# Performance work log

Measured on AMD Instinct MI355X. Metric: run time of the kernel, lower is better.

The kernel has to match this reference:

```python
import jax, jax.numpy as jnp
import numpy as np

NUM_GROUPS = 32
EPS = 1e-5

def group_norm(x, gamma, beta):
    # x: [B, C, L]
    B, C, L = x.shape
    g = x.reshape(B, NUM_GROUPS, C // NUM_GROUPS, L)
    mu = g.mean(axis=(2, 3), keepdims=True)
    var = g.var(axis=(2, 3), keepdims=True)
    g = (g - mu) * jax.lax.rsqrt(var + EPS)
    h = g.reshape(B, C, L)
    return h * gamma[None, :, None] + beta[None, :, None]

def conv1x1(h, W, b):
    # h: [B, C, L], W: [Cout, Cin], b: [Cout] -> [B, Cout, L]
    return jnp.einsum('oc,bcl->bol', W, h) + b[None, :, None]

def setup_inputs() -> dict:
    key = jax.random.key(0)
    ks = jax.random.split(key, 10)
    B, C, L = 8, 512, 2048
    s = 1.0 / np.sqrt(C)
    inp = {
        'x': jax.random.normal(ks[0], (B, C, L), dtype=jnp.float32),
        'gn_gamma': jnp.ones((C,), jnp.float32),
        'gn_beta': jnp.zeros((C,), jnp.float32),
        'Wq': jax.random.normal(ks[1], (C, C), jnp.float32) * s,
        'bq': jnp.zeros((C,), jnp.float32),
        'Wk': jax.random.normal(ks[2], (C, C), jnp.float32) * s,
        'bk': jnp.zeros((C,), jnp.float32),
        'Wv': jax.random.normal(ks[3], (C, C), jnp.float32) * s,
        'bv': jnp.zeros((C,), jnp.float32),
        'Wo': jax.random.normal(ks[4], (C, C), jnp.float32) * s,
        'bo': jnp.zeros((C,), jnp.float32),
    }
    return inp

def reference(x, gn_gamma, gn_beta, Wq, bq, Wk, bk, Wv, bv, Wo, bo):
    B, C, L = x.shape
    h = group_norm(x, gn_gamma, gn_beta)
    q = conv1x1(h, Wq, bq)  # [B, C, L]
    k = conv1x1(h, Wk, bk)  # [B, C, L]
    v = conv1x1(h, Wv, bv)  # [B, C, L]
    scale = 1.0 / jnp.sqrt(jnp.float32(C)).astype(x.dtype)
    w = jnp.einsum('bci,bcj->bij', q, k) * scale  # [B, L, L]
    w = jax.nn.softmax(w, axis=-1)
    a = jnp.einsum('bij,bcj->bci', w, v)  # [B, C, L]
    return x + conv1x1(a, Wo, bo)
```

## Files before the change

kernel.cpp:

```cpp
#include <hip/hip_runtime.h>
#include <hip/hip_bf16.h>

#define B_ 8
#define C_ 512
#define L_ 2048
#define G_ 32

typedef __attribute__((ext_vector_type(8))) short bf16x8;
typedef __attribute__((ext_vector_type(4))) float f32x4;

__device__ __forceinline__ float b2f(short h) {
    union { unsigned u; float f; } c; c.u = ((unsigned)(unsigned short)h) << 16; return c.f;
}
__device__ __forceinline__ short f2b(float f) {
    union { float f; unsigned u; } c; c.f = f;
    unsigned r = (c.u + 0x7FFFu + ((c.u >> 16) & 1u)) >> 16;
    return (short)r;
}

__device__ __forceinline__ void load_lds16(const void* g, void* s) {
    __builtin_amdgcn_global_load_lds(
        (const __attribute__((address_space(1))) void*)g,
        (__attribute__((address_space(3))) void*)s, 16, 0, 0);
}

template<int N>
__device__ __forceinline__ void wait_vm() {
    if constexpr (N == 0)      asm volatile("s_waitcnt vmcnt(0)" ::: "memory");
    else if constexpr (N == 6) asm volatile("s_waitcnt vmcnt(6)" ::: "memory");
    else                       asm volatile("s_waitcnt vmcnt(8)" ::: "memory");
    __builtin_amdgcn_sched_barrier(0);
}
__device__ __forceinline__ void sbar() {
    __builtin_amdgcn_sched_barrier(0);
    __builtin_amdgcn_s_barrier();
    __builtin_amdgcn_sched_barrier(0);
}

__global__ __launch_bounds__(256) void cvt_w(
    const float* __restrict__ a, const float* __restrict__ b,
    const float* __restrict__ c, const float* __restrict__ d,
    short* __restrict__ o)
{
    const float* src = (blockIdx.y == 0) ? a : (blockIdx.y == 1) ? b
                     : (blockIdx.y == 2) ? c : d;
    short* dst = o + (size_t)blockIdx.y * (C_ * C_);
    int i = (blockIdx.x * 256 + threadIdx.x) * 4;
    float4 v = *(const float4*)(src + i);
    short4 r;
    r.x = f2b(v.x); r.y = f2b(v.y); r.z = f2b(v.z); r.w = f2b(v.w);
    *(short4*)(dst + i) = r;
}

__global__ __launch_bounds__(256) void groupnorm_tr(
    const float* __restrict__ x, const float* __restrict__ gamma,
    const float* __restrict__ beta, short* __restrict__ h_t,
    float* __restrict__ rsum)
{
    int bg = blockIdx.x;
    int b = bg >> 5, g = bg & 31;
    const float* xg = x + ((size_t)b * C_ + (size_t)g * 16) * L_;
    int t = threadIdx.x;
    if (t < 64) rsum[(size_t)bg * 64 + t] = 0.f;
    float s = 0.f, ss = 0.f;
    for (int i = t; i < 8192; i += 256) {
        float4 v = ((const float4*)xg)[i];
        s  += v.x + v.y + v.z + v.w;
        ss += v.x * v.x + v.y * v.y + v.z * v.z + v.w * v.w;
    }
    #pragma unroll
    for (int o = 32; o > 0; o >>= 1) { s += __shfl_down(s, o); ss += __shfl_down(ss, o); }
    __shared__ float rs[4], rss[4], stats[2], gam[16], bet[16];
    int wave = t >> 6, lane = t & 63;
    if (lane == 0) { rs[wave] = s; rss[wave] = ss; }
    if (t < 16) { gam[t] = gamma[g * 16 + t]; bet[t] = beta[g * 16 + t]; }
    __syncthreads();
    if (t == 0) {
        float S = rs[0] + rs[1] + rs[2] + rs[3];
        float SS = rss[0] + rss[1] + rss[2] + rss[3];
        float mean = S * (1.f / 32768.f);
        float var = SS * (1.f / 32768.f) - mean * mean;
        stats[0] = mean; stats[1] = rsqrtf(var + 1e-5f);
    }
    __syncthreads();
    float mean = stats[0], rstd = stats[1];
    short* ho = h_t + (size_t)b * L_ * C_ + (size_t)g * 16;
    for (int i = t; i < 32768; i += 256) {
        int cl = i & 15, l = i >> 4;
        float xv = xg[cl * L_ + l];
        float hv = (xv - mean) * rstd * gam[cl] + bet[cl];
        ho[(size_t)l * C_ + cl] = f2b(hv);
    }
}

template<int BM, int PIPE, int BIAS_MODE, bool RESID, bool OUTF32, bool EXPSUM, bool ROWDIV>
__global__ __launch_bounds__(BM * 2) void gemm_bt(
    const short* __restrict__ A, const short* __restrict__ Bt,
    void* __restrict__ Co, const float* __restrict__ bias,
    const float* __restrict__ bias2, const float* __restrict__ resid,
    float* __restrict__ rowsum,
    int N, int K, int lda, int ldb, int ldc,
    long sA, long sB, long sC, float alpha)
{
    constexpr int T = BM * 2;
    constexpr int RPP = T / 8;
    constexpr int LPS = BM / RPP + 128 / RPP;
    constexpr int NBUF = (PIPE == 1) ? 2 : 1;
    __shared__ __align__(16) short As[NBUF][BM * 64];
    __shared__ __align__(16) short Bs[NBUF][128 * 64];

    int nbx = gridDim.x, nby = gridDim.y, nbz = gridDim.z;
    int lin = blockIdx.x + nbx * (blockIdx.y + nby * blockIdx.z);
    int total = nbx * nby * nbz;
    int bx, by, bz;
    if ((total & 7) == 0) {
        int chunk = total >> 3;
        int logical = (lin & 7) * chunk + (lin >> 3);
        bx = logical % nbx; int t2 = logical / nbx; by = t2 % nby; bz = t2 / nby;
    } else { bx = blockIdx.x; by = blockIdx.y; bz = blockIdx.z; }

    const short* Ab = A + (size_t)bz * sA;
    const short* Bb = Bt + (size_t)bz * sB;
    int m0 = by * BM, n0 = bx * 128;
    int t = threadIdx.x, lane = t & 63;
    int wave = t >> 6;
    int wm = wave >> 1, wn = wave & 1;

    f32x4 acc[4][4] = {};

    int rs_ = t >> 3, cs_ = t & 7;
    int gcol = ((cs_ ^ (rs_ & 7)) << 3);
    const short* gA = Ab + (size_t)(m0 + rs_) * lda + gcol;
    const short* gB = Bb + (size_t)(n0 + rs_) * ldb + gcol;
    int fr = lane & 15, fq = lane >> 4;
    int ch0 = (fq ^ (fr & 7)) << 3;
    int ch1 = ((4 | fq) ^ (fr & 7)) << 3;

    auto stage = [&](short* Asb, short* Bsb) {
        #pragma unroll
        for (int i = 0; i < BM / RPP; i++)
            load_lds16(gA + (size_t)(RPP * i) * lda, Asb + i * (RPP * 64) + t * 8);
        #pragma unroll
        for (int i = 0; i < 128 / RPP; i++)
            load_lds16(gB + (size_t)(RPP * i) * ldb, Bsb + i * (RPP * 64) + t * 8);
        gA += 64; gB += 64;
    };
    auto compute = [&](const short* Asb, const short* Bsb) {
        #pragma unroll
        for (int kk = 0; kk < 2; kk++) {
            int ch = kk ? ch1 : ch0;
            bf16x8 af[4], bfr[4];
            #pragma unroll
            for (int i = 0; i < 4; i++) {
                int R = wm * 64 + i * 16 + fr;
                af[i] = *(const bf16x8*)(Asb + R * 64 + ch);
            }
            #pragma unroll
            for (int j = 0; j < 4; j++) {
                int R = wn * 64 + j * 16 + fr;
                bfr[j] = *(const bf16x8*)(Bsb + R * 64 + ch);
            }
            #pragma unroll
            for (int mt = 0; mt < 4; mt++)
                #pragma unroll
                for (int nt = 0; nt < 4; nt++)
                    acc[mt][nt] = __builtin_amdgcn_mfma_f32_16x16x32_bf16(
                        af[mt], bfr[nt], acc[mt][nt], 0, 0, 0);
        }
    };

    if constexpr (PIPE == 0) {
        for (int k0 = 0; k0 < K; k0 += 64) {
            __syncthreads();
            stage(As[0], Bs[0]);
            __syncthreads();
            compute(As[0], Bs[0]);
        }
    } else {
        int nk = K >> 6;
        stage(As[0], Bs[0]);
        stage(As[1], Bs[1]);
        wait_vm<LPS>();
        sbar();
        for (int kt = 0; kt < nk; kt += 2) {
            compute(As[0], Bs[0]);
            sbar();
            if (kt + 2 < nk) { stage(As[0], Bs[0]); wait_vm<LPS>(); }
            else               wait_vm<0>();
            sbar();
            compute(As[1], Bs[1]);
            sbar();
            if (kt + 3 < nk) { stage(As[1], Bs[1]); wait_vm<LPS>(); }
            else               wait_vm<0>();
            sbar();
        }
    }

    size_t cb = (size_t)bz * sC;
    int crow = (lane >> 4) * 4;
    int wrow = wm * 64;
    float psum[4][4];
    float inv[4][4];
    if (EXPSUM) {
        #pragma unroll
        for (int mt = 0; mt < 4; mt++)
            #pragma unroll
            for (int r = 0; r < 4; r++) psum[mt][r] = 0.f;
    }
    if (ROWDIV) {
        #pragma unroll
        for (int mt = 0; mt < 4; mt++)
            #pragma unroll
            for (int r = 0; r < 4; r++) {
                int m = m0 + wrow + mt * 16 + crow + r;
                inv[mt][r] = 1.f / rowsum[(size_t)bz * L_ + m];
            }
    }
    #pragma unroll
    for (int mt = 0; mt < 4; mt++) {
        #pragma unroll
        for (int nt = 0; nt < 4; nt++) {
            int n = n0 + wn * 64 + nt * 16 + fr;
            float bn = 0.f;
            if (BIAS_MODE == 3) bn = (n < 512) ? bias[n] : bias2[n - 512];
            #pragma unroll
            for (int r = 0; r < 4; r++) {
                int m = m0 + wrow + mt * 16 + crow + r;
                float v = acc[mt][nt][r] * alpha;
                if (EXPSUM) { v = __expf(v); psum[mt][r] += v; }
                if (ROWDIV) v *= inv[mt][r];
                if (BIAS_MODE == 3) v += bn;
                if (BIAS_MODE == 2) v += bias[m];
                size_t idx = cb + (size_t)m * ldc + n;
                if (RESID) v += resid[idx];
                if (OUTF32) ((float*)Co)[idx] = v;
                else        ((short*)Co)[idx] = f2b(v);
            }
        }
    }
    if (EXPSUM) {
        #pragma unroll
        for (int mt = 0; mt < 4; mt++)
            #pragma unroll
            for (int r = 0; r < 4; r++) {
                float s = psum[mt][r];
                s += __shfl_xor(s, 1); s += __shfl_xor(s, 2);
                s += __shfl_xor(s, 4); s += __shfl_xor(s, 8);
                if ((lane & 15) == 0) {
                    int m = m0 + wrow + mt * 16 + crow + r;
                    atomicAdd(rowsum + (size_t)bz * L_ + m, s);
                }
            }
    }
}

extern "C" void kernel_launch(void* const* d_in, const int* in_sizes, int n_in,
                              void* d_out, int out_size, void* d_ws, size_t ws_size,
                              hipStream_t stream)
{
    const float* x     = (const float*)d_in[0];
    const float* gamma = (const float*)d_in[1];
    const float* beta  = (const float*)d_in[2];
    const float* Wq    = (const float*)d_in[3];
    const float* bq    = (const float*)d_in[4];
    const float* Wk    = (const float*)d_in[5];
    const float* bk    = (const float*)d_in[6];
    const float* Wv    = (const float*)d_in[7];
    const float* bv    = (const float*)d_in[8];
    const float* Wo    = (const float*)d_in[9];
    const float* bo    = (const float*)d_in[10];
    float* out = (float*)d_out;

    const size_t MiB = 1024 * 1024;
    const size_t CC = (size_t)C_ * C_;
    const size_t LC = (size_t)L_ * C_;
    const size_t LL = (size_t)L_ * L_;
    const size_t wbytes = 4 * CC * sizeof(short);

    const size_t perb = 16 * MiB + L_ * sizeof(float);
    int nb = 1;
    for (int c = 8; c >= 1; c >>= 1)
        if (ws_size >= wbytes + (size_t)c * perb) { nb = c; break; }

    short* wq_b = (short*)d_ws;
    short* wv_b = wq_b + 2 * CC;
    short* wo_b = wv_b + CC;
    short* h_t  = wo_b + CC;
    short* qk_t = h_t + (size_t)nb * LC;
    short* v_   = qk_t + (size_t)nb * 2 * LC;
    short* S    = v_  + (size_t)nb * LC;
    float* rsum = (float*)(S + (size_t)nb * LL);
    short* a_t  = h_t;

    const long sLC = (long)LC;
    const long sLL = (long)LL;
    const float scale = 0.044194173824159216f;

    cvt_w<<<dim3(C_ * C_ / 1024, 4), 256, 0, stream>>>(Wq, Wk, Wv, Wo, wq_b);

    for (int b0 = 0; b0 < B_; b0 += nb) {
        const float* xb = x + (size_t)b0 * LC;
        float* outb = out + (size_t)b0 * LC;

        groupnorm_tr<<<dim3(nb * G_), 256, 0, stream>>>(xb, gamma, beta, h_t, rsum);

        gemm_bt<128, 1, 3, false, false, false, false><<<dim3(8, 16, nb), 256, 0, stream>>>(
            h_t, wq_b, qk_t, bq, bk, nullptr, nullptr,
            1024, 512, 512, 512, 1024, sLC, 0, 2 * sLC, 1.f);
        gemm_bt<128, 1, 2, false, false, false, false><<<dim3(16, 4, nb), 256, 0, stream>>>(
            wv_b, h_t, v_, bv, nullptr, nullptr, nullptr,
            2048, 512, 512, 512, 2048, 0, sLC, sLC, 1.f);
        gemm_bt<256, 0, 0, false, false, true, false><<<dim3(16, 8, nb), 512, 0, stream>>>(
            qk_t, qk_t + 512, S, nullptr, nullptr, nullptr, rsum,
            2048, 512, 1024, 1024, 2048, 2 * sLC, 2 * sLC, sLL, scale);
        gemm_bt<128, 1, 0, false, false, false, true><<<dim3(4, 16, nb), 256, 0, stream>>>(
            S, v_, a_t, nullptr, nullptr, nullptr, rsum,
            512, 2048, 2048, 2048, 512, sLL, sLC, sLC, 1.f);
        gemm_bt<128, 1, 2, true, true, false, false><<<dim3(16, 4, nb), 256, 0, stream>>>(
            wo_b, a_t, outb, bo, nullptr, xb, nullptr,
            2048, 512, 512, 512, 2048, 0, sLC, sLC, 1.f);
    }
}
```

Baseline: 303.7 us.

## Add 256x256 8-wave pipelined GEMM kernel for QK projection and scores

Adds a new gemm8 kernel with 256x256 tiles, 8 waves, double-buffered LDS staging interleaved with MFMA sub-blocks, setprio hints and an XCD-aware block remap. It replaces the generic gemm_bt for the fused Q/K projection and for the QK^T score GEMM with fused exp and row-sum. The goal is more reuse per tile and better overlap of global-to-LDS loads with matrix math. The cost is higher register and LDS pressure (128KB LDS per block) and fewer blocks for the smaller projection GEMM.

Result: no change. 300.3 us (-1.1%).

```diff
diff --git a/kernel.cpp b/kernel.cpp
--- a/kernel.cpp
+++ b/kernel.cpp
@@ -27,8 +27,13 @@
 template<int N>
 __device__ __forceinline__ void wait_vm() {
     if constexpr (N == 0)      asm volatile("s_waitcnt vmcnt(0)" ::: "memory");
+    else if constexpr (N == 2) asm volatile("s_waitcnt vmcnt(2)" ::: "memory");
     else if constexpr (N == 6) asm volatile("s_waitcnt vmcnt(6)" ::: "memory");
     else                       asm volatile("s_waitcnt vmcnt(8)" ::: "memory");
+    __builtin_amdgcn_sched_barrier(0);
+}
+__device__ __forceinline__ void wait_lgkm0() {
+    asm volatile("s_waitcnt lgkmcnt(0)" ::: "memory");
     __builtin_amdgcn_sched_barrier(0);
 }
 __device__ __forceinline__ void sbar() {
@@ -90,6 +95,157 @@
         float xv = xg[cl * L_ + l];
         float hv = (xv - mean) * rstd * gam[cl] + bet[cl];
         ho[(size_t)l * C_ + cl] = f2b(hv);
+    }
+}
+
+#define MM(mh, nh, bfx)                                                        \
+  do {                                                                         \
+    _Pragma("unroll") for (int i_ = 0; i_ < 4; i_++)                           \
+    _Pragma("unroll") for (int j_ = 0; j_ < 2; j_++)                           \
+    _Pragma("unroll") for (int kk_ = 0; kk_ < 2; kk_++)                        \
+      acc[(mh)*4 + i_][(nh)*2 + j_] = __builtin_amdgcn_mfma_f32_16x16x32_bf16( \
+          af[i_][kk_], bfx[j_][kk_], acc[(mh)*4 + i_][(nh)*2 + j_], 0, 0, 0);  \
+  } while (0)
+
+template<int BIAS_MODE, bool EXPSUM>
+__global__ __launch_bounds__(512, 2) void gemm8(
+    const short* __restrict__ A, const short* __restrict__ Bt,
+    void* __restrict__ Co, const float* __restrict__ bias,
+    const float* __restrict__ bias2, float* __restrict__ rowsum,
+    int K, int lda, int ldb, int ldc,
+    long sA, long sB, long sC, float alpha)
+{
+    __shared__ __align__(16) short As0[256 * 64];
+    __shared__ __align__(16) short As1[256 * 64];
+    __shared__ __align__(16) short Bs0[256 * 64];
+    __shared__ __align__(16) short Bs1[256 * 64];
+
+    int nbx = gridDim.x, nby = gridDim.y, nbz = gridDim.z;
+    int lin = blockIdx.x + nbx * (blockIdx.y + nby * blockIdx.z);
+    int total = nbx * nby * nbz;
+    int bx, by, bz;
+    if ((total & 7) == 0) {
+        int chunk = total >> 3;
+        int logical = (lin & 7) * chunk + (lin >> 3);
+        bx = logical % nbx; int t2 = logical / nbx; by = t2 % nby; bz = t2 / nby;
+    } else { bx = blockIdx.x; by = blockIdx.y; bz = blockIdx.z; }
+
+    int m0 = by * 256, n0 = bx * 256;
+    int t = threadIdx.x, lane = t & 63;
+    int wave = t >> 6;
+    int wm = wave >> 2, wn = wave & 3;
+    int fr = lane & 15, fq = lane >> 4;
+    int ch0 = (fq ^ (fr & 7)) << 3;
+    int ch1 = ((4 | fq) ^ (fr & 7)) << 3;
+    int rs_ = t >> 3, cs_ = t & 7;
+    int gcol = ((cs_ ^ (rs_ & 7)) << 3);
+
+    const short* gA = A + (size_t)bz * sA + (size_t)(m0 + rs_) * lda + gcol;
+    const short* gB = Bt + (size_t)bz * sB + (size_t)(n0 + rs_) * ldb + gcol;
+
+    f32x4 acc[8][4] = {};
+    bf16x8 af[4][2], bf0[2][2], bf1[2][2];
+
+    auto stgA = [&](short* dst, int tile, int h) {
+        const short* s = gA + (size_t)(h * 128) * lda + tile * 64;
+        load_lds16(s, dst + h * 8192 + t * 8);
+        load_lds16(s + (size_t)64 * lda, dst + h * 8192 + 4096 + t * 8);
+    };
+    auto stgB = [&](short* dst, int tile, int h) {
+        const short* s = gB + (size_t)(h * 128) * ldb + tile * 64;
+        load_lds16(s, dst + h * 8192 + t * 8);
+        load_lds16(s + (size_t)64 * ldb, dst + h * 8192 + 4096 + t * 8);
+    };
+    auto rdA = [&](const short* S, int mh) {
+        #pragma unroll
+        for (int i = 0; i < 4; i++) {
+            int R = wm * 128 + (mh * 4 + i) * 16 + fr;
+            af[i][0] = *(const bf16x8*)(S + R * 64 + ch0);
+            af[i][1] = *(const bf16x8*)(S + R * 64 + ch1);
+        }
+    };
+    auto rdB = [&](const short* S, int nh, bf16x8 (&bf)[2][2]) {
+        #pragma unroll
+        for (int j = 0; j < 2; j++) {
+            int R = wn * 64 + (nh * 2 + j) * 16 + fr;
+            bf[j][0] = *(const bf16x8*)(S + R * 64 + ch0);
+            bf[j][1] = *(const bf16x8*)(S + R * 64 + ch1);
+        }
+    };
+
+    int nk = K >> 6;
+
+    auto TILE = [&](short* cA, short* cB, short* nA, short* nB, int tt) {
+        rdA(cA, 0); rdB(cB, 0, bf0);
+        if (tt + 1 < nk) stgA(nA, tt + 1, 1);
+        sbar(); wait_lgkm0();
+        __builtin_amdgcn_s_setprio(1); MM(0, 0, bf0); __builtin_amdgcn_s_setprio(0);
+        sbar();
+        rdB(cB, 1, bf1);
+        if (tt + 1 < nk) stgB(nB, tt + 1, 0);
+        sbar(); wait_lgkm0();
+        __builtin_amdgcn_s_setprio(1); MM(0, 1, bf1); __builtin_amdgcn_s_setprio(0);
+        sbar();
+        rdA(cA, 1);
+        if (tt + 1 < nk) stgB(nB, tt + 1, 1);
+        sbar(); wait_lgkm0();
+        __builtin_amdgcn_s_setprio(1); MM(1, 0, bf0); __builtin_amdgcn_s_setprio(0);
+        sbar();
+        if (tt + 2 < nk) stgA(cA, tt + 2, 0);
+        __builtin_amdgcn_s_setprio(1); MM(1, 1, bf1); __builtin_amdgcn_s_setprio(0);
+        if (tt + 2 < nk) wait_vm<2>(); else wait_vm<0>();
+        sbar();
+    };
+
+    stgA(As0, 0, 0); stgA(As0, 0, 1); stgB(Bs0, 0, 0); stgB(Bs0, 0, 1);
+    if (nk > 1) stgA(As1, 1, 0);
+    wait_vm<2>();
+    sbar();
+
+    for (int tt = 0; tt < nk; tt += 2) {
+        TILE(As0, Bs0, As1, Bs1, tt);
+        TILE(As1, Bs1, As0, Bs0, tt + 1);
+    }
+
+    size_t cb = (size_t)bz * sC;
+    int crow = fq * 4;
+    float psum[8][4];
+    if (EXPSUM) {
+        #pragma unroll
+        for (int mi = 0; mi < 8; mi++)
+            #pragma unroll
+            for (int r = 0; r < 4; r++) psum[mi][r] = 0.f;
+    }
+    #pragma unroll
+    for (int mi = 0; mi < 8; mi++) {
+        #pragma unroll
+        for (int nj = 0; nj < 4; nj++) {
+            int n = n0 + wn * 64 + nj * 16 + fr;
+            float bn = 0.f;
+            if (BIAS_MODE == 3) bn = (n < 512) ? bias[n] : bias2[n - 512];
+            #pragma unroll
+            for (int r = 0; r < 4; r++) {
+                int m = m0 + wm * 128 + mi * 16 + crow + r;
+                float v = acc[mi][nj][r] * alpha;
+                if (EXPSUM) { v = __expf(v); psum[mi][r] += v; }
+                if (BIAS_MODE == 3) v += bn;
+                ((short*)Co)[cb + (size_t)m * ldc + n] = f2b(v);
+            }
+        }
+    }
+    if (EXPSUM) {
+        #pragma unroll
+        for (int mi = 0; mi < 8; mi++)
+            #pragma unroll
+            for (int r = 0; r < 4; r++) {
+                float s = psum[mi][r];
+                s += __shfl_xor(s, 1); s += __shfl_xor(s, 2);
+                s += __shfl_xor(s, 4); s += __shfl_xor(s, 8);
+                if ((lane & 15) == 0) {
+                    int m = m0 + wm * 128 + mi * 16 + crow + r;
+                    atomicAdd(rowsum + (size_t)bz * L_ + m, s);
+                }
+            }
     }
 }
 
@@ -304,15 +460,15 @@
 
         groupnorm_tr<<<dim3(nb * G_), 256, 0, stream>>>(xb, gamma, beta, h_t, rsum);
 
-        gemm_bt<128, 1, 3, false, false, false, false><<<dim3(8, 16, nb), 256, 0, stream>>>(
-            h_t, wq_b, qk_t, bq, bk, nullptr, nullptr,
-            1024, 512, 512, 512, 1024, sLC, 0, 2 * sLC, 1.f);
+        gemm8<3, false><<<dim3(4, 8, nb), 512, 0, stream>>>(
+            h_t, wq_b, qk_t, bq, bk, nullptr,
+            512, 512, 512, 1024, sLC, 0, 2 * sLC, 1.f);
         gemm_bt<128, 1, 2, false, false, false, false><<<dim3(16, 4, nb), 256, 0, stream>>>(
             wv_b, h_t, v_, bv, nullptr, nullptr, nullptr,
             2048, 512, 512, 512, 2048, 0, sLC, sLC, 1.f);
-        gemm_bt<256, 0, 0, false, false, true, false><<<dim3(16, 8, nb), 512, 0, stream>>>(
-            qk_t, qk_t + 512, S, nullptr, nullptr, nullptr, rsum,
-            2048, 512, 1024, 1024, 2048, 2 * sLC, 2 * sLC, sLL, scale);
+        gemm8<0, true><<<dim3(8, 8, nb), 512, 0, stream>>>(
+            qk_t, qk_t + 512, S, nullptr, nullptr, rsum,
+            512, 1024, 1024, 2048, 2 * sLC, 2 * sLC, sLL, scale);
         gemm_bt<128, 1, 0, false, false, false, true><<<dim3(4, 16, nb), 256, 0, stream>>>(
             S, v_, a_t, nullptr, nullptr, nullptr, rsum,
             512, 2048, 2048, 2048, 512, sLL, sLC, sLC, 1.f);
```

## Fuse QK^T scores and V projection into one launch, stage groupnorm via LDS

Applied to the files above, without the earlier changes.

The QK^T score GEMM (with exp and row-sum) and the V projection GEMM now run as tiles of a single kernel launch, with an interleaved block-to-tile mapping. This removes one launch and lets the two independent GEMMs fill the device together. Groupnorm now caches the group's input in shared memory during the statistics pass, so the second pass reads LDS instead of re-reading global memory, and it writes packed bf16 pairs. The exp uses exp2 with a pre-folded log2e scale, and the Q/K projection switches to 256-row tiles without double buffering, which may lower occupancy or overlap.

New measurement: 275.7 us. -9.2%, faster.

```diff
diff --git a/kernel.cpp b/kernel.cpp
--- a/kernel.cpp
+++ b/kernel.cpp
@@ -9,9 +9,6 @@
 typedef __attribute__((ext_vector_type(8))) short bf16x8;
 typedef __attribute__((ext_vector_type(4))) float f32x4;
 
-__device__ __forceinline__ float b2f(short h) {
-    union { unsigned u; float f; } c; c.u = ((unsigned)(unsigned short)h) << 16; return c.f;
-}
 __device__ __forceinline__ short f2b(float f) {
     union { float f; unsigned u; } c; c.f = f;
     unsigned r = (c.u + 0x7FFFu + ((c.u >> 16) & 1u)) >> 16;
@@ -27,7 +24,6 @@
 template<int N>
 __device__ __forceinline__ void wait_vm() {
     if constexpr (N == 0)      asm volatile("s_waitcnt vmcnt(0)" ::: "memory");
-    else if constexpr (N == 6) asm volatile("s_waitcnt vmcnt(6)" ::: "memory");
     else                       asm volatile("s_waitcnt vmcnt(8)" ::: "memory");
     __builtin_amdgcn_sched_barrier(0);
 }
@@ -57,20 +53,24 @@
     const float* __restrict__ beta, short* __restrict__ h_t,
     float* __restrict__ rsum)
 {
+    __shared__ float xb[16][2052];
+    __shared__ float rs[4], rss[4], stats[2], gam[16], bet[16];
     int bg = blockIdx.x;
     int b = bg >> 5, g = bg & 31;
     const float* xg = x + ((size_t)b * C_ + (size_t)g * 16) * L_;
     int t = threadIdx.x;
     if (t < 64) rsum[(size_t)bg * 64 + t] = 0.f;
     float s = 0.f, ss = 0.f;
+    #pragma unroll 4
     for (int i = t; i < 8192; i += 256) {
         float4 v = ((const float4*)xg)[i];
+        int cl = i >> 9, l4 = (i & 511) << 2;
+        *(float4*)&xb[cl][l4] = v;
         s  += v.x + v.y + v.z + v.w;
         ss += v.x * v.x + v.y * v.y + v.z * v.z + v.w * v.w;
     }
     #pragma unroll
     for (int o = 32; o > 0; o >>= 1) { s += __shfl_down(s, o); ss += __shfl_down(ss, o); }
-    __shared__ float rs[4], rss[4], stats[2], gam[16], bet[16];
     int wave = t >> 6, lane = t & 63;
     if (lane == 0) { rs[wave] = s; rss[wave] = ss; }
     if (t < 16) { gam[t] = gamma[g * 16 + t]; bet[t] = beta[g * 16 + t]; }
@@ -85,15 +85,135 @@
     __syncthreads();
     float mean = stats[0], rstd = stats[1];
     short* ho = h_t + (size_t)b * L_ * C_ + (size_t)g * 16;
-    for (int i = t; i < 32768; i += 256) {
-        int cl = i & 15, l = i >> 4;
-        float xv = xg[cl * L_ + l];
-        float hv = (xv - mean) * rstd * gam[cl] + bet[cl];
-        ho[(size_t)l * C_ + cl] = f2b(hv);
-    }
-}
-
-template<int BM, int PIPE, int BIAS_MODE, bool RESID, bool OUTF32, bool EXPSUM, bool ROWDIV>
+    for (int i = t; i < 16384; i += 256) {
+        int cp = (i & 7) * 2, l = i >> 3;
+        float a0 = (xb[cp][l]     - mean) * rstd * gam[cp]     + bet[cp];
+        float a1 = (xb[cp + 1][l] - mean) * rstd * gam[cp + 1] + bet[cp + 1];
+        unsigned pk = (unsigned)(unsigned short)f2b(a0)
+                    | ((unsigned)(unsigned short)f2b(a1) << 16);
+        *(unsigned*)(ho + (size_t)l * C_ + cp) = pk;
+    }
+}
+
+__global__ __launch_bounds__(512) void qk_vproj(
+    const short* __restrict__ qk, const short* __restrict__ ht,
+    const short* __restrict__ wv, short* __restrict__ S,
+    short* __restrict__ v_, const float* __restrict__ bv,
+    float* __restrict__ rsum, int nb, float alpha2)
+{
+    __shared__ __align__(16) short As[256 * 64];
+    __shared__ __align__(16) short Bs[128 * 64];
+    const int LC = L_ * C_;
+    const size_t LL = (size_t)L_ * L_;
+
+    int total = nb * 160;
+    int lin = blockIdx.x;
+    int chunk = total >> 3;
+    int logical = (lin & 7) * chunk + (lin >> 3);
+    int qkN = nb << 7;
+    bool isQK = logical < qkN;
+    int bz, bx, by;
+    if (isQK) { bz = logical >> 7; int rr = logical & 127; bx = rr & 15; by = rr >> 4; }
+    else      { int r = logical - qkN; bz = r >> 5; int rr = r & 31; bx = rr & 15; by = rr >> 4; }
+
+    int m0 = by * 256, n0 = bx * 128;
+    int lda = isQK ? 1024 : 512;
+    const short* Ab = isQK ? qk + (size_t)bz * (2 * LC) : wv;
+    const short* Bb = isQK ? qk + 512 + (size_t)bz * (2 * LC) : ht + (size_t)bz * LC;
+
+    int t = threadIdx.x, lane = t & 63, wave = t >> 6;
+    int wm = wave >> 1, wn = wave & 1;
+    f32x4 acc[4][4] = {};
+
+    int rs_ = t >> 3, cs_ = t & 7;
+    int gcol = (cs_ ^ (rs_ & 7)) << 3;
+    const short* gA = Ab + (size_t)(m0 + rs_) * lda + gcol;
+    const short* gB = Bb + (size_t)(n0 + rs_) * lda + gcol;
+    int fr = lane & 15, fq = lane >> 4;
+    int ch0 = (fq ^ (fr & 7)) << 3, ch1 = ((4 | fq) ^ (fr & 7)) << 3;
+
+    for (int k0 = 0; k0 < 512; k0 += 64) {
+        __syncthreads();
+        #pragma unroll
+        for (int i = 0; i < 4; i++)
+            load_lds16(gA + (size_t)(64 * i) * lda, As + i * 4096 + t * 8);
+        #pragma unroll
+        for (int i = 0; i < 2; i++)
+            load_lds16(gB + (size_t)(64 * i) * lda, Bs + i * 4096 + t * 8);
+        gA += 64; gB += 64;
+        __syncthreads();
+        #pragma unroll
+        for (int kk = 0; kk < 2; kk++) {
+            int ch = kk ? ch1 : ch0;
+            bf16x8 af[4], bfr[4];
+            #pragma unroll
+            for (int i = 0; i < 4; i++)
+                af[i] = *(const bf16x8*)(As + (wm * 64 + i * 16 + fr) * 64 + ch);
+            #pragma unroll
+            for (int j = 0; j < 4; j++)
+                bfr[j] = *(const bf16x8*)(Bs + (wn * 64 + j * 16 + fr) * 64 + ch);
+            #pragma unroll
+            for (int mt = 0; mt < 4; mt++)
+                #pragma unroll
+                for (int nt = 0; nt < 4; nt++)
+                    acc[mt][nt] = __builtin_amdgcn_mfma_f32_16x16x32_bf16(
+                        af[mt], bfr[nt], acc[mt][nt], 0, 0, 0);
+        }
+    }
+
+    int crow = fq * 4, wrow = wm * 64;
+    if (isQK) {
+        short* Co = S + (size_t)bz * LL;
+        float psum[4][4];
+        #pragma unroll
+        for (int mt = 0; mt < 4; mt++)
+            #pragma unroll
+            for (int r = 0; r < 4; r++) psum[mt][r] = 0.f;
+        #pragma unroll
+        for (int mt = 0; mt < 4; mt++) {
+            #pragma unroll
+            for (int nt = 0; nt < 4; nt++) {
+                int n = n0 + wn * 64 + nt * 16 + fr;
+                #pragma unroll
+                for (int r = 0; r < 4; r++) {
+                    int m = m0 + wrow + mt * 16 + crow + r;
+                    float v = exp2f(acc[mt][nt][r] * alpha2);
+                    psum[mt][r] += v;
+                    Co[(size_t)m * L_ + n] = f2b(v);
+                }
+            }
+        }
+        #pragma unroll
+        for (int mt = 0; mt < 4; mt++)
+            #pragma unroll
+            for (int r = 0; r < 4; r++) {
+                float s = psum[mt][r];
+                s += __shfl_xor(s, 1); s += __shfl_xor(s, 2);
+                s += __shfl_xor(s, 4); s += __shfl_xor(s, 8);
+                if ((lane & 15) == 0) {
+                    int m = m0 + wrow + mt * 16 + crow + r;
+                    atomicAdd(rsum + (size_t)bz * L_ + m, s);
+                }
+            }
+    } else {
+        short* Co = v_ + (size_t)bz * LC;
+        #pragma unroll
+        for (int mt = 0; mt < 4; mt++) {
+            #pragma unroll
+            for (int nt = 0; nt < 4; nt++) {
+                int n = n0 + wn * 64 + nt * 16 + fr;
+                #pragma unroll
+                for (int r = 0; r < 4; r++) {
+                    int m = m0 + wrow + mt * 16 + crow + r;
+                    float v = acc[mt][nt][r] + bv[m];
+                    Co[(size_t)m * L_ + n] = f2b(v);
+                }
+            }
+        }
+    }
+}
+
+template<int BM, int PIPE, int BIAS_MODE, bool RESID, bool OUTF32, bool ROWDIV>
 __global__ __launch_bounds__(BM * 2) void gemm_bt(
     const short* __restrict__ A, const short* __restrict__ Bt,
     void* __restrict__ Co, const float* __restrict__ bias,
@@ -151,15 +271,11 @@
             int ch = kk ? ch1 : ch0;
             bf16x8 af[4], bfr[4];
             #pragma unroll
-            for (int i = 0; i < 4; i++) {
-                int R = wm * 64 + i * 16 + fr;
-                af[i] = *(const bf16x8*)(Asb + R * 64 + ch);
-            }
-            #pragma unroll
-            for (int j = 0; j < 4; j++) {
-                int R = wn * 64 + j * 16 + fr;
-                bfr[j] = *(const bf16x8*)(Bsb + R * 64 + ch);
-            }
+            for (int i = 0; i < 4; i++)
+                af[i] = *(const bf16x8*)(Asb + (wm * 64 + i * 16 + fr) * 64 + ch);
+            #pragma unroll
+            for (int j = 0; j < 4; j++)
+                bfr[j] = *(const bf16x8*)(Bsb + (wn * 64 + j * 16 + fr) * 64 + ch);
             #pragma unroll
             for (int mt = 0; mt < 4; mt++)
                 #pragma unroll
@@ -199,14 +315,7 @@
     size_t cb = (size_t)bz * sC;
     int crow = (lane >> 4) * 4;
     int wrow = wm * 64;
-    float psum[4][4];
     float inv[4][4];
-    if (EXPSUM) {
-        #pragma unroll
-        for (int mt = 0; mt < 4; mt++)
-            #pragma unroll
-            for (int r = 0; r < 4; r++) psum[mt][r] = 0.f;
-    }
     if (ROWDIV) {
         #pragma unroll
         for (int mt = 0; mt < 4; mt++)
@@ -227,7 +336,6 @@
             for (int r = 0; r < 4; r++) {
                 int m = m0 + wrow + mt * 16 + crow + r;
                 float v = acc[mt][nt][r] * alpha;
-                if (EXPSUM) { v = __expf(v); psum[mt][r] += v; }
                 if (ROWDIV) v *= inv[mt][r];
                 if (BIAS_MODE == 3) v += bn;
                 if (BIAS_MODE == 2) v += bias[m];
@@ -237,20 +345,6 @@
                 else        ((short*)Co)[idx] = f2b(v);
             }
         }
-    }
-    if (EXPSUM) {
-        #pragma unroll
-        for (int mt = 0; mt < 4; mt++)
-            #pragma unroll
-            for (int r = 0; r < 4; r++) {
-                float s = psum[mt][r];
-                s += __shfl_xor(s, 1); s += __shfl_xor(s, 2);
-                s += __shfl_xor(s, 4); s += __shfl_xor(s, 8);
-                if ((lane & 15) == 0) {
-                    int m = m0 + wrow + mt * 16 + crow + r;
-                    atomicAdd(rowsum + (size_t)bz * L_ + m, s);
-                }
-            }
     }
 }
 
@@ -294,7 +388,7 @@
 
     const long sLC = (long)LC;
     const long sLL = (long)LL;
-    const float scale = 0.044194173824159216f;
+    const float alpha2 = 0.04419417382415922f * 1.4426950408889634f;
 
     cvt_w<<<dim3(C_ * C_ / 1024, 4), 256, 0, stream>>>(Wq, Wk, Wv, Wo, wq_b);
 
@@ -304,19 +398,15 @@
 
         groupnorm_tr<<<dim3(nb * G_), 256, 0, stream>>>(xb, gamma, beta, h_t, rsum);
 
-        gemm_bt<128, 1, 3, false, false, false, false><<<dim3(8, 16, nb), 256, 0, stream>>>(
+        gemm_bt<256, 0, 3, false, false, false><<<dim3(8, 8, nb), 512, 0, stream>>>(
             h_t, wq_b, qk_t, bq, bk, nullptr, nullptr,
             1024, 512, 512, 512, 1024, sLC, 0, 2 * sLC, 1.f);
-        gemm_bt<128, 1, 2, false, false, false, false><<<dim3(16, 4, nb), 256, 0, stream>>>(
-            wv_b, h_t, v_, bv, nullptr, nullptr, nullptr,
-            2048, 512, 512, 512, 2048, 0, sLC, sLC, 1.f);
-        gemm_bt<256, 0, 0, false, false, true, false><<<dim3(16, 8, nb), 512, 0, stream>>>(
-            qk_t, qk_t + 512, S, nullptr, nullptr, nullptr, rsum,
-            2048, 512, 1024, 1024, 2048, 2 * sLC, 2 * sLC, sLL, scale);
-        gemm_bt<128, 1, 0, false, false, false, true><<<dim3(4, 16, nb), 256, 0, stream>>>(
+        qk_vproj<<<dim3(nb * 160), 512, 0, stream>>>(
+            qk_t, h_t, wv_b, S, v_, bv, rsum, nb, alpha2);
+        gemm_bt<128, 1, 0, false, false, true><<<dim3(4, 16, nb), 256, 0, stream>>>(
             S, v_, a_t, nullptr, nullptr, nullptr, rsum,
             512, 2048, 2048, 2048, 512, sLL, sLC, sLC, 1.f);
-        gemm_bt<128, 1, 2, true, true, false, false><<<dim3(16, 4, nb), 256, 0, stream>>>(
+        gemm_bt<128, 1, 2, true, true, false><<<dim3(16, 4, nb), 256, 0, stream>>>(
             wo_b, a_t, outb, bo, nullptr, xb, nullptr,
             2048, 512, 512, 512, 2048, 0, sLC, sLC, 1.f);
     }
```
